# Optimization experiments

Hardware: AMD Instinct MI355X
Metric: run time of the kernel (lower is better)

## Reference

```python
import jax, jax.numpy as jnp
import numpy as np
import math

NFEAT = 1024
NHID = 512
NLAYERS = 8
LAMDA = 0.5
ALPHA = 0.1
N_DIA = 48
DIA_L = 64
N = N_DIA * DIA_L


def setup_inputs() -> dict:
    key = jax.random.key(0)
    ks = jax.random.split(key, 16)
    stdv_fc = 1.0 / math.sqrt(NFEAT)
    stdv_gc = 1.0 / math.sqrt(NHID)
    inp = {
        'a': jax.random.normal(ks[0], (N, NFEAT), jnp.float32),
        'v': jax.random.normal(ks[1], (N, NFEAT), jnp.float32),
        'l': jax.random.normal(ks[2], (N, NFEAT), jnp.float32),
        'W0': jax.random.uniform(ks[3], (NFEAT, NHID), jnp.float32, -stdv_fc, stdv_fc),
        'b0': jax.random.uniform(ks[4], (NHID,), jnp.float32, -stdv_fc, stdv_fc),
        'W1': jax.random.uniform(ks[5], (NFEAT, NHID), jnp.float32, -stdv_fc, stdv_fc),
        'b1': jax.random.uniform(ks[6], (NHID,), jnp.float32, -stdv_fc, stdv_fc),
        'W2': jax.random.uniform(ks[7], (NFEAT, NHID), jnp.float32, -stdv_fc, stdv_fc),
        'b2': jax.random.uniform(ks[8], (NHID,), jnp.float32, -stdv_fc, stdv_fc),
        'Wconv': jax.random.uniform(ks[9], (NLAYERS, NHID, NHID), jnp.float32, -stdv_gc, stdv_gc),
        'dia_len': DIA_L,  # uniform dialogue length
        'topicLabel': jnp.zeros((N,), jnp.int64),
    }
    return inp


def create_big_adj(a, v, l, dia_l):
    n = a.shape[0]
    d = n // dia_l
    feats = jnp.stack([a, v, l])                    # [3, N, F]
    x = feats.reshape(3, d, dia_l, -1)              # [3, D, L, F]
    nrm = x / jnp.sqrt(jnp.sum(x * x, axis=-1, keepdims=True))
    cos = jnp.einsum('mdif,mdjf->mdij', nrm, nrm) * 0.99999
    sim = jnp.arccos(cos)                           # [3, D, L, L]
    adj = jnp.zeros((3 * n, 3 * n), dtype=a.dtype)
    base = jnp.arange(d)[:, None, None] * dia_l     # dialogue start offsets
    rows = jnp.broadcast_to(base + jnp.arange(dia_l)[:, None], (d, dia_l, dia_l))
    cols = jnp.broadcast_to(base + jnp.arange(dia_l)[None, :], (d, dia_l, dia_l))
    for m in range(3):  # same-modality block-diagonal acos-similarity blocks
        adj = adj.at[m * n + rows, m * n + cols].set(sim[m])
    k = jnp.arange(n)
    for m in range(3):  # cross-modal: same-utterance links set to 0.99999
        for mm in range(3):
            if m != mm:
                adj = adj.at[m * n + k, mm * n + k].set(0.99999)
    dsum = jnp.sum(adj, axis=1)
    dinv = dsum ** -0.5
    return dinv[:, None] * adj * dinv[None, :]


def reference(a, v, l, W0, b0, W1, b1, W2, b2, Wconv, dia_len, topicLabel):
    relu = jax.nn.relu
    # eval mode: dropout is identity
    a_ = relu(a @ W0 + b0)
    l_ = relu(l @ W1 + b1)
    v_ = relu(v @ W2 + b2)
    x = jnp.concatenate([a_, v_, l_], axis=0)       # [3N, nhidden]
    adj = create_big_adj(a, v, l, dia_len)
    h0 = x
    h = x
    for i in range(NLAYERS):
        theta = math.log(LAMDA / (i + 1) + 1.0)
        hi = adj @ h
        support = (1.0 - ALPHA) * hi + ALPHA * h0
        h = relu(theta * (support @ Wconv[i]) + (1.0 - theta) * support)
    n = a.shape[0]
    out = jnp.concatenate([h[:n], h[n:2 * n], h[2 * n:]], axis=-1)  # [N, 3*nhidden]
    out = jnp.concatenate([l, out], axis=-1)        # use_residue
    return out
```

## Files before the change

### kernel.cpp

```cpp
#include <hip/hip_runtime.h>
#include <hip/hip_bf16.h>
#include <cmath>

#define NFEAT 1024
#define NHID  512
#define NLAYERS 8
#define NDIA 48
#define DIAL 64
#define NROW (NDIA*DIAL)
#define NROW3 (3*NROW)

typedef short bf16x8 __attribute__((ext_vector_type(8)));
typedef float f32x4  __attribute__((ext_vector_type(4)));
typedef unsigned short u16x8 __attribute__((ext_vector_type(8)));
typedef unsigned short u16x4 __attribute__((ext_vector_type(4)));
typedef unsigned short ushort_t;

__device__ __forceinline__ unsigned short f2bf(float x) {
  __hip_bfloat16 h = __float2bfloat16(x);
  return __builtin_bit_cast(unsigned short, h);
}
__device__ __forceinline__ float bf2f(unsigned short u) {
  __hip_bfloat16 h = __builtin_bit_cast(__hip_bfloat16, u);
  return __bfloat162float(h);
}

__device__ __forceinline__ void gload16(const void* g, void* l) {
  __builtin_amdgcn_global_load_lds(
      (const __attribute__((address_space(1))) void*)g,
      (__attribute__((address_space(3))) void*)l, 16, 0, 0);
}

__global__ __launch_bounds__(256) void k_prep(const float* __restrict__ a, const float* __restrict__ v,
                      const float* __restrict__ l, ushort_t* __restrict__ Abuf,
                      float* __restrict__ invn) {
  int gid = blockIdx.x * 256 + threadIdx.x;
  int row = gid >> 6, lane = gid & 63;
  int m = row / NROW, r = row % NROW;
  const float* src = (m == 0 ? a : (m == 1 ? v : l)) + (size_t)r * NFEAT;
  float4 x[4];
  float s = 0.f;
#pragma unroll
  for (int q = 0; q < 4; ++q) {
    x[q] = *reinterpret_cast<const float4*>(src + lane * 4 + q * 256);
    s += x[q].x*x[q].x + x[q].y*x[q].y + x[q].z*x[q].z + x[q].w*x[q].w;
  }
#pragma unroll
  for (int off = 32; off; off >>= 1) s += __shfl_xor(s, off);
  if (lane == 0) invn[row] = rsqrtf(s);
  ushort_t* da = Abuf + (size_t)row * NFEAT;
#pragma unroll
  for (int q = 0; q < 4; ++q) {
    u16x4 oa;
    oa[0] = f2bf(x[q].x); oa[1] = f2bf(x[q].y); oa[2] = f2bf(x[q].z); oa[3] = f2bf(x[q].w);
    *reinterpret_cast<u16x4*>(da + lane * 4 + q * 256) = oa;
  }
}

__global__ __launch_bounds__(256) void k_simm(const ushort_t* __restrict__ Ab,
                      const float* __restrict__ invn,
                      ushort_t* __restrict__ Sbf, float* __restrict__ dinv) {
  __shared__ short Xs[2][4096];
  __shared__ float simS[64][73];
  __shared__ float invS[64];
  int blk = blockIdx.x;
  const ushort_t* Xb = Ab + (size_t)blk * 64 * NFEAT;
  int t = threadIdx.x, w = t >> 6, lane = t & 63;
  if (t < 64) invS[t] = invn[blk * 64 + t];
  f32x4 acc[4] = {};

#define STAGE_SIM(b, k0) do { \
    _Pragma("unroll") \
    for (int q = 0; q < 2; ++q) { \
      int f_ = t * 8 + q * 2048; \
      int row_ = f_ >> 6; \
      int col_ = (f_ & 63) ^ ((row_ & 7) << 3); \
      gload16(Xb + (size_t)row_ * NFEAT + (k0) + col_, (void*)(Xs[b] + q * 2048 + w * 512)); \
    } } while (0)

  STAGE_SIM(0, 0);
  __syncthreads();
  for (int it = 0; it < 16; ++it) {
    int cur = it & 1;
    if (it < 15) STAGE_SIM(cur ^ 1, (it + 1) * 64);
    const char* base = (const char*)Xs[cur];
#pragma unroll
    for (int ks = 0; ks < 2; ++ks) {
      int koff = ks * 32 + (lane >> 4) * 8;
      int arow = w * 16 + (lane & 15);
      bf16x8 af = *(const bf16x8*)(base + (((arow << 7) + (koff << 1)) ^ ((arow & 7) << 4)));
#pragma unroll
      for (int j = 0; j < 4; ++j) {
        int brow = j * 16 + (lane & 15);
        bf16x8 bf = *(const bf16x8*)(base + (((brow << 7) + (koff << 1)) ^ ((brow & 7) << 4)));
        acc[j] = __builtin_amdgcn_mfma_f32_16x16x32_bf16(af, bf, acc[j], 0, 0, 0);
      }
    }
    __syncthreads();
  }
#undef STAGE_SIM

#pragma unroll
  for (int j = 0; j < 4; ++j)
#pragma unroll
    for (int e = 0; e < 4; ++e) {
      int r = w * 16 + (lane >> 4) * 4 + e;
      int c = j * 16 + (lane & 15);
      float cc = acc[j][e] * invS[r] * invS[c] * 0.99999f;
      cc = fminf(fmaxf(cc, -0.99999f), 0.99999f);
      simS[r][c] = acosf(cc);
    }
  __syncthreads();
  if (t < 64) {
    float s = 0.f;
#pragma unroll 8
    for (int c = 0; c < 64; ++c) s += simS[t][c];
    float di = rsqrtf(s + 1.99998f);
    simS[t][64] = di;
    dinv[blk * 64 + t] = di;
  }
  __syncthreads();
  ushort_t* Sb = Sbf + (size_t)blk * 4096;
#pragma unroll
  for (int q = 0; q < 2; ++q) {
    int idx = t * 8 + q * 2048;
    int i = idx >> 6, j0 = idx & 63;
    float di = simS[i][64];
    u16x8 o;
#pragma unroll
    for (int e = 0; e < 8; ++e)
      o[e] = f2bf(simS[i][j0 + e] * di * simS[j0 + e][64]);
    *reinterpret_cast<u16x8*>(Sb + idx) = o;
  }
}

__global__ void k_cvt_w(const float* __restrict__ s0, const float* __restrict__ s1,
                        const float* __restrict__ s2, ushort_t* __restrict__ dst,
                        int K, int mode) {
  __shared__ float tile[32][33];
  int z = blockIdx.z;
  const float* src = (mode == 1) ? (s0 + (size_t)z * K * NHID)
                                 : (z == 0 ? s0 : (z == 1 ? s1 : s2));
  ushort_t* d = dst + (size_t)z * NHID * K;
  int n0 = blockIdx.x * 32, k0 = blockIdx.y * 32;
  int tx = threadIdx.x & 31, ty = threadIdx.x >> 5;
#pragma unroll
  for (int q = 0; q < 4; ++q)
    tile[ty + q * 8][tx] = src[(size_t)(k0 + ty + q * 8) * NHID + n0 + tx];
  __syncthreads();
#pragma unroll
  for (int q = 0; q < 4; ++q)
    d[(size_t)(n0 + ty + q * 8) * K + k0 + tx] = f2bf(tile[tx][ty + q * 8]);
}

template<int EPI>
__global__ __launch_bounds__(256) void k_gemm_mfma(
    const ushort_t* __restrict__ A, const ushort_t* __restrict__ B,
    const float* __restrict__ ba, const float* __restrict__ bv, const float* __restrict__ bl,
    const ushort_t* __restrict__ sup, ushort_t* __restrict__ C, ushort_t* __restrict__ C2,
    int K, float theta) {
  __shared__ short As[2][128 * 64];
  __shared__ short Bs[2][64 * 64];
  int t = threadIdx.x;
  int w = t >> 6, lane = t & 63;
  int bm = blockIdx.x * 128, bn = blockIdx.y * 64;
  const float* bias = ba;
  if (EPI == 0) {
    int band = bm / NROW;
    B += (size_t)band * NHID * K;
    bias = (band == 0 ? ba : (band == 1 ? bv : bl));
  }
  const ushort_t* Ab = A + (size_t)bm * K;
  const ushort_t* Bb = B + (size_t)bn * K;
  int wr = (w >> 1) * 64, wc = (w & 1) * 32;
  f32x4 acc[4][2] = {};

#define STAGE_G(b, k0) do { \
    _Pragma("unroll") \
    for (int q = 0; q < 4; ++q) { \
      int f_ = t * 8 + q * 2048; int row_ = f_ >> 6; \
      int col_ = (f_ & 63) ^ ((row_ & 7) << 3); \
      gload16(Ab + (size_t)row_ * K + (k0) + col_, (void*)(As[b] + q * 2048 + w * 512)); } \
    _Pragma("unroll") \
    for (int q = 0; q < 2; ++q) { \
      int f_ = t * 8 + q * 2048; int row_ = f_ >> 6; \
      int col_ = (f_ & 63) ^ ((row_ & 7) << 3); \
      gload16(Bb + (size_t)row_ * K + (k0) + col_, (void*)(Bs[b] + q * 2048 + w * 512)); } \
  } while (0)

  STAGE_G(0, 0);
  __syncthreads();
  int T = K >> 6;
  for (int s = 0; s < T; ++s) {
    int cur = s & 1;
    if (s + 1 < T) STAGE_G(cur ^ 1, (s + 1) * 64);
    const char* ab = (const char*)As[cur];
    const char* bb = (const char*)Bs[cur];
#pragma unroll
    for (int ks = 0; ks < 2; ++ks) {
      bf16x8 af[4], bfr[2];
#pragma unroll
      for (int i = 0; i < 4; ++i) {
        int arow = wr + i * 16 + (lane & 15);
        int abo = (arow << 7) + ((ks * 32 + (lane >> 4) * 8) << 1);
        af[i] = *reinterpret_cast<const bf16x8*>(ab + (abo ^ ((arow & 7) << 4)));
      }
#pragma unroll
      for (int j = 0; j < 2; ++j) {
        int brow = wc + j * 16 + (lane & 15);
        int bbo = (brow << 7) + ((ks * 32 + (lane >> 4) * 8) << 1);
        bfr[j] = *reinterpret_cast<const bf16x8*>(bb + (bbo ^ ((brow & 7) << 4)));
      }
#pragma unroll
      for (int i = 0; i < 4; ++i)
#pragma unroll
        for (int j = 0; j < 2; ++j)
          acc[i][j] = __builtin_amdgcn_mfma_f32_16x16x32_bf16(af[i], bfr[j], acc[i][j], 0, 0, 0);
    }
    __syncthreads();
  }
#undef STAGE_G

#pragma unroll
  for (int i = 0; i < 4; ++i) {
#pragma unroll
    for (int jf = 0; jf < 2; ++jf) {
      int r0 = bm + wr + i * 16 + (lane >> 4) * 4;
      int c  = bn + wc + jf * 16 + (lane & 15);
#pragma unroll
      for (int j = 0; j < 4; ++j) {
        int r = r0 + j;
        float val = acc[i][jf][j];
        if (EPI == 0) {
          val = fmaxf(val + bias[c], 0.f);
          unsigned short o = f2bf(val);
          C[(size_t)r * NHID + c] = o;
          C2[(size_t)r * NHID + c] = o;
        } else {
          float s = bf2f(sup[(size_t)r * NHID + c]);
          val = fmaxf(theta * val + (1.f - theta) * s, 0.f);
          C[(size_t)r * NHID + c] = f2bf(val);
        }
      }
    }
  }
}

__global__ __launch_bounds__(256) void k_adj(const ushort_t* __restrict__ Sbf,
                      const ushort_t* __restrict__ h, const ushort_t* __restrict__ h0,
                      const float* __restrict__ dinv, ushort_t* __restrict__ sup) {
  __shared__ char ldsb[52224];
  short* Ss = (short*)ldsb;
  short (*Ht)[72] = (short (*)[72])(ldsb + 24576);
  float (*supF)[68] = (float (*)[68])ldsb;
  int d = blockIdx.x, c0 = blockIdx.y * 64;
  int t = threadIdx.x, w = t >> 6, lane = t & 63;
#pragma unroll
  for (int q = 0; q < 6; ++q) {
    int f = t * 8 + q * 2048;
    int mod = f >> 12, rem = f & 4095;
    int row = rem >> 6;
    int col = (rem & 63) ^ ((row & 7) << 3);
    gload16(Sbf + ((size_t)(mod * NDIA + d)) * 4096 + row * 64 + col,
            (void*)(Ss + q * 2048 + w * 512));
  }
#pragma unroll
  for (int q = 0; q < 6; ++q) {
    int idx = t + q * 256;
    int mod = idx >> 9, rem = idx & 511;
    int j = rem >> 3, n0 = (rem & 7) * 8;
    int key = rem & 7;
    u16x8 hv = *reinterpret_cast<const u16x8*>(
        h + ((size_t)(mod * NROW + d * 64 + j)) * NHID + c0 + n0);
    int js = j ^ (key << 3);
#pragma unroll
    for (int e = 0; e < 8; ++e) Ht[mod * 64 + n0 + e][js] = hv[e];
  }
  __syncthreads();
  f32x4 acc[3][4] = {};
#pragma unroll
  for (int m = 0; m < 3; ++m)
#pragma unroll
    for (int ks = 0; ks < 2; ++ks) {
      int koff = ks * 32 + (lane >> 4) * 8;
      int arow = w * 16 + (lane & 15);
      bf16x8 af = *(const bf16x8*)((const char*)Ss + m * 8192 +
                    (((arow << 7) + (koff << 1)) ^ ((arow & 7) << 4)));
#pragma unroll
      for (int j = 0; j < 4; ++j) {
        int n = j * 16 + (lane & 15);
        int koff_s = koff ^ (((n >> 3) & 7) << 3);
        bf16x8 bf = *(const bf16x8*)(&Ht[m * 64 + n][koff_s]);
        acc[m][j] = __builtin_amdgcn_mfma_f32_16x16x32_bf16(af, bf, acc[m][j], 0, 0, 0);
      }
    }
  __syncthreads();
#pragma unroll
  for (int m = 0; m < 3; ++m)
#pragma unroll
    for (int j = 0; j < 4; ++j)
#pragma unroll
      for (int e = 0; e < 4; ++e)
        supF[m * 64 + w * 16 + (lane >> 4) * 4 + e][j * 16 + (lane & 15)] = acc[m][j][e];
  __syncthreads();
  int r = t >> 2, cc0 = (t & 3) * 16;
  int u = d * 64 + r;
  float dv[3] = {dinv[u], dinv[NROW + u], dinv[2 * NROW + u]};
#pragma unroll
  for (int m = 0; m < 3; ++m) {
    int mm1 = (m + 1) % 3, mm2 = (m + 2) % 3;
    int g = m * NROW + u;
    float c1 = 0.99999f * dv[m] * dv[mm1];
    float c2 = 0.99999f * dv[m] * dv[mm2];
    const ushort_t* p1 = h + ((size_t)(mm1 * NROW + u)) * NHID + c0 + cc0;
    const ushort_t* p2 = h + ((size_t)(mm2 * NROW + u)) * NHID + c0 + cc0;
    const ushort_t* pz = h0 + (size_t)g * NHID + c0 + cc0;
    ushort_t* po = sup + (size_t)g * NHID + c0 + cc0;
#pragma unroll
    for (int half = 0; half < 2; ++half) {
      u16x8 h1 = *reinterpret_cast<const u16x8*>(p1 + half * 8);
      u16x8 h2 = *reinterpret_cast<const u16x8*>(p2 + half * 8);
      u16x8 hz = *reinterpret_cast<const u16x8*>(pz + half * 8);
      u16x8 o;
#pragma unroll
      for (int e = 0; e < 8; ++e) {
        float val = 0.9f * (supF[m * 64 + r][cc0 + half * 8 + e]
                    + c1 * bf2f(h1[e]) + c2 * bf2f(h2[e]))
                  + 0.1f * bf2f(hz[e]);
        o[e] = f2bf(val);
      }
      *reinterpret_cast<u16x8*>(po + half * 8) = o;
    }
  }
}

__global__ void k_out(const float* __restrict__ l, const ushort_t* __restrict__ h,
                      float* __restrict__ out) {
  int idx = blockIdx.x * blockDim.x + threadIdx.x;
  int i = idx / 640;
  int c4 = (idx % 640) * 4;
  float4 val;
  if (c4 < 1024) {
    val = *reinterpret_cast<const float4*>(l + (size_t)i * NFEAT + c4);
  } else {
    int cc = c4 - 1024;
    int m = cc >> 9, c = cc & 511;
    u16x4 hv = *reinterpret_cast<const u16x4*>(h + ((size_t)m * NROW + i) * NHID + c);
    val.x = bf2f(hv[0]); val.y = bf2f(hv[1]); val.z = bf2f(hv[2]); val.w = bf2f(hv[3]);
  }
  *reinterpret_cast<float4*>(out + (size_t)i * 2560 + c4) = val;
}

extern "C" void kernel_launch(void* const* d_in, const int* in_sizes, int n_in,
                              void* d_out, int out_size, void* d_ws, size_t ws_size,
                              hipStream_t stream) {
  const float* a  = (const float*)d_in[0];
  const float* v  = (const float*)d_in[1];
  const float* l  = (const float*)d_in[2];
  const float* W0 = (const float*)d_in[3];
  const float* b0 = (const float*)d_in[4];
  const float* W1 = (const float*)d_in[5];
  const float* b1 = (const float*)d_in[6];
  const float* W2 = (const float*)d_in[7];
  const float* b2 = (const float*)d_in[8];
  const float* Wc = (const float*)d_in[9];
  float* out = (float*)d_out;

  const size_t SZ = (size_t)NROW3 * NHID;
  const size_t XSZ = (size_t)3 * NROW * NFEAT;
  char* ws = (char*)d_ws;
  ushort_t* Abuf = (ushort_t*)ws;  ws += XSZ * 2;
  ushort_t* h0   = (ushort_t*)ws;  ws += SZ * 2;
  ushort_t* h    = (ushort_t*)ws;  ws += SZ * 2;
  ushort_t* sup  = (ushort_t*)ws;  ws += SZ * 2;
  ushort_t* Wtfc = (ushort_t*)ws;  ws += (size_t)3 * NHID * NFEAT * 2;
  ushort_t* Wct  = (ushort_t*)ws;  ws += (size_t)NLAYERS * NHID * NHID * 2;
  ushort_t* Sbf  = (ushort_t*)ws;  ws += (size_t)144 * 4096 * 2;
  float* dinv    = (float*)ws;     ws += (size_t)NROW3 * 4;
  float* invn    = (float*)ws;

  k_prep<<<NROW3 / 4, 256, 0, stream>>>(a, v, l, Abuf, invn);
  k_cvt_w<<<dim3(NHID / 32, NFEAT / 32, 3), 256, 0, stream>>>(W0, W2, W1, Wtfc, NFEAT, 0);
  k_cvt_w<<<dim3(NHID / 32, NHID / 32, NLAYERS), 256, 0, stream>>>(Wc, nullptr, nullptr, Wct, NHID, 1);
  k_simm<<<3 * NDIA, 256, 0, stream>>>(Abuf, invn, Sbf, dinv);

  k_gemm_mfma<0><<<dim3(NROW3 / 128, NHID / 64), 256, 0, stream>>>(
      Abuf, Wtfc, b0, b2, b1, nullptr, h0, h, NFEAT, 0.f);

  for (int i = 0; i < NLAYERS; ++i) {
    float theta = (float)std::log(0.5 / (i + 1) + 1.0);
    k_adj<<<dim3(NDIA, NHID / 64), 256, 0, stream>>>(Sbf, h, h0, dinv, sup);
    k_gemm_mfma<1><<<dim3(NROW3 / 128, NHID / 64), 256, 0, stream>>>(
        sup, Wct + (size_t)i * NHID * NHID, nullptr, nullptr, nullptr, sup, h, nullptr, NHID, theta);
  }

  k_out<<<(NROW * 2560 / 4) / 256, 256, 0, stream>>>(l, h, out);
}
```

Before: 229.7 us.

## Use smaller 64x64 tiles for per-layer GEMM and prefetch adj epilogue loads

Splits the templated GEMM into a dedicated FC kernel and a new per-layer GEMM with 64x64 tiles, so the 9216x512x512 layer GEMM launches twice as many blocks (1152 instead of 576) for better occupancy across CUs. In the adjacency kernel, the global loads for the cross-modal and h0 residual terms are issued before the MFMA phase, so their latency overlaps with compute. The cost is more register pressure from the prefetched vectors, and lower per-block data reuse in the smaller GEMM tiles.

```diff
diff --git a/kernel.cpp b/kernel.cpp
--- a/kernel.cpp
+++ b/kernel.cpp
@@ -153,23 +153,19 @@
     d[(size_t)(n0 + ty + q * 8) * K + k0 + tx] = f2bf(tile[tx][ty + q * 8]);
 }
 
-template<int EPI>
-__global__ __launch_bounds__(256) void k_gemm_mfma(
+__global__ __launch_bounds__(256) void k_fc(
     const ushort_t* __restrict__ A, const ushort_t* __restrict__ B,
     const float* __restrict__ ba, const float* __restrict__ bv, const float* __restrict__ bl,
-    const ushort_t* __restrict__ sup, ushort_t* __restrict__ C, ushort_t* __restrict__ C2,
-    int K, float theta) {
+    ushort_t* __restrict__ C, ushort_t* __restrict__ C2) {
   __shared__ short As[2][128 * 64];
   __shared__ short Bs[2][64 * 64];
+  const int K = NFEAT;
   int t = threadIdx.x;
   int w = t >> 6, lane = t & 63;
   int bm = blockIdx.x * 128, bn = blockIdx.y * 64;
-  const float* bias = ba;
-  if (EPI == 0) {
-    int band = bm / NROW;
-    B += (size_t)band * NHID * K;
-    bias = (band == 0 ? ba : (band == 1 ? bv : bl));
-  }
+  int band = bm / NROW;
+  B += (size_t)band * NHID * K;
+  const float* bias = (band == 0 ? ba : (band == 1 ? bv : bl));
   const ushort_t* Ab = A + (size_t)bm * K;
   const ushort_t* Bb = B + (size_t)bn * K;
   int wr = (w >> 1) * 64, wc = (w & 1) * 32;
@@ -190,7 +186,7 @@
 
   STAGE_G(0, 0);
   __syncthreads();
-  int T = K >> 6;
+  const int T = K >> 6;
   for (int s = 0; s < T; ++s) {
     int cur = s & 1;
     if (s + 1 < T) STAGE_G(cur ^ 1, (s + 1) * 64);
@@ -230,18 +226,75 @@
 #pragma unroll
       for (int j = 0; j < 4; ++j) {
         int r = r0 + j;
-        float val = acc[i][jf][j];
-        if (EPI == 0) {
-          val = fmaxf(val + bias[c], 0.f);
-          unsigned short o = f2bf(val);
-          C[(size_t)r * NHID + c] = o;
-          C2[(size_t)r * NHID + c] = o;
-        } else {
-          float s = bf2f(sup[(size_t)r * NHID + c]);
-          val = fmaxf(theta * val + (1.f - theta) * s, 0.f);
-          C[(size_t)r * NHID + c] = f2bf(val);
-        }
-      }
+        float val = fmaxf(acc[i][jf][j] + bias[c], 0.f);
+        unsigned short o = f2bf(val);
+        C[(size_t)r * NHID + c] = o;
+        C2[(size_t)r * NHID + c] = o;
+      }
+    }
+  }
+}
+
+__global__ __launch_bounds__(256) void k_gemm2(
+    const ushort_t* __restrict__ A, const ushort_t* __restrict__ B,
+    const ushort_t* __restrict__ sup_ep, ushort_t* __restrict__ C, float theta) {
+  __shared__ short As[2][64 * 64];
+  __shared__ short Bs[2][64 * 64];
+  const int K = NHID;
+  int t = threadIdx.x, w = t >> 6, lane = t & 63;
+  int bm = blockIdx.x * 64, bn = blockIdx.y * 64;
+  const ushort_t* Ab = A + (size_t)bm * K;
+  const ushort_t* Bb = B + (size_t)bn * K;
+  f32x4 acc[4] = {};
+
+#define STAGE_2(b, k0) do { \
+    _Pragma("unroll") \
+    for (int q = 0; q < 2; ++q) { \
+      int f_ = t * 8 + q * 2048; int row_ = f_ >> 6; \
+      int col_ = (f_ & 63) ^ ((row_ & 7) << 3); \
+      gload16(Ab + (size_t)row_ * K + (k0) + col_, (void*)(As[b] + q * 2048 + w * 512)); } \
+    _Pragma("unroll") \
+    for (int q = 0; q < 2; ++q) { \
+      int f_ = t * 8 + q * 2048; int row_ = f_ >> 6; \
+      int col_ = (f_ & 63) ^ ((row_ & 7) << 3); \
+      gload16(Bb + (size_t)row_ * K + (k0) + col_, (void*)(Bs[b] + q * 2048 + w * 512)); } \
+  } while (0)
+
+  STAGE_2(0, 0);
+  __syncthreads();
+  const int T = K >> 6;
+  for (int s = 0; s < T; ++s) {
+    int cur = s & 1;
+    if (s + 1 < T) STAGE_2(cur ^ 1, (s + 1) * 64);
+    const char* ab = (const char*)As[cur];
+    const char* bb = (const char*)Bs[cur];
+#pragma unroll
+    for (int ks = 0; ks < 2; ++ks) {
+      int koff = ks * 32 + (lane >> 4) * 8;
+      int arow = w * 16 + (lane & 15);
+      bf16x8 af = *(const bf16x8*)(ab + (((arow << 7) + (koff << 1)) ^ ((arow & 7) << 4)));
+#pragma unroll
+      for (int j = 0; j < 4; ++j) {
+        int brow = j * 16 + (lane & 15);
+        bf16x8 bfr = *(const bf16x8*)(bb + (((brow << 7) + (koff << 1)) ^ ((brow & 7) << 4)));
+        acc[j] = __builtin_amdgcn_mfma_f32_16x16x32_bf16(af, bfr, acc[j], 0, 0, 0);
+      }
+    }
+    __syncthreads();
+  }
+#undef STAGE_2
+
+  float omt = 1.f - theta;
+#pragma unroll
+  for (int j = 0; j < 4; ++j) {
+    int c = bn + j * 16 + (lane & 15);
+    int r0 = bm + w * 16 + (lane >> 4) * 4;
+#pragma unroll
+    for (int e = 0; e < 4; ++e) {
+      int r = r0 + e;
+      float sv = bf2f(sup_ep[(size_t)r * NHID + c]);
+      float val = fmaxf(theta * acc[j][e] + omt * sv, 0.f);
+      C[(size_t)r * NHID + c] = f2bf(val);
     }
   }
 }
@@ -276,6 +329,23 @@
 #pragma unroll
     for (int e = 0; e < 8; ++e) Ht[mod * 64 + n0 + e][js] = hv[e];
   }
+  int r = t >> 2, cc0 = (t & 3) * 16;
+  int u = d * 64 + r;
+  float dv[3] = {dinv[u], dinv[NROW + u], dinv[2 * NROW + u]};
+  u16x8 pre[3][3][2];
+#pragma unroll
+  for (int m = 0; m < 3; ++m) {
+    int mm1 = (m + 1) % 3, mm2 = (m + 2) % 3;
+    const ushort_t* p1 = h + ((size_t)(mm1 * NROW + u)) * NHID + c0 + cc0;
+    const ushort_t* p2 = h + ((size_t)(mm2 * NROW + u)) * NHID + c0 + cc0;
+    const ushort_t* pz = h0 + ((size_t)(m * NROW + u)) * NHID + c0 + cc0;
+    pre[m][0][0] = *reinterpret_cast<const u16x8*>(p1);
+    pre[m][0][1] = *reinterpret_cast<const u16x8*>(p1 + 8);
+    pre[m][1][0] = *reinterpret_cast<const u16x8*>(p2);
+    pre[m][1][1] = *reinterpret_cast<const u16x8*>(p2 + 8);
+    pre[m][2][0] = *reinterpret_cast<const u16x8*>(pz);
+    pre[m][2][1] = *reinterpret_cast<const u16x8*>(pz + 8);
+  }
   __syncthreads();
   f32x4 acc[3][4] = {};
 #pragma unroll
@@ -303,30 +373,21 @@
       for (int e = 0; e < 4; ++e)
         supF[m * 64 + w * 16 + (lane >> 4) * 4 + e][j * 16 + (lane & 15)] = acc[m][j][e];
   __syncthreads();
-  int r = t >> 2, cc0 = (t & 3) * 16;
-  int u = d * 64 + r;
-  float dv[3] = {dinv[u], dinv[NROW + u], dinv[2 * NROW + u]};
 #pragma unroll
   for (int m = 0; m < 3; ++m) {
     int mm1 = (m + 1) % 3, mm2 = (m + 2) % 3;
     int g = m * NROW + u;
     float c1 = 0.99999f * dv[m] * dv[mm1];
     float c2 = 0.99999f * dv[m] * dv[mm2];
-    const ushort_t* p1 = h + ((size_t)(mm1 * NROW + u)) * NHID + c0 + cc0;
-    const ushort_t* p2 = h + ((size_t)(mm2 * NROW + u)) * NHID + c0 + cc0;
-    const ushort_t* pz = h0 + (size_t)g * NHID + c0 + cc0;
     ushort_t* po = sup + (size_t)g * NHID + c0 + cc0;
 #pragma unroll
     for (int half = 0; half < 2; ++half) {
-      u16x8 h1 = *reinterpret_cast<const u16x8*>(p1 + half * 8);
-      u16x8 h2 = *reinterpret_cast<const u16x8*>(p2 + half * 8);
-      u16x8 hz = *reinterpret_cast<const u16x8*>(pz + half * 8);
       u16x8 o;
 #pragma unroll
       for (int e = 0; e < 8; ++e) {
         float val = 0.9f * (supF[m * 64 + r][cc0 + half * 8 + e]
-                    + c1 * bf2f(h1[e]) + c2 * bf2f(h2[e]))
-                  + 0.1f * bf2f(hz[e]);
+                    + c1 * bf2f(pre[m][0][half][e]) + c2 * bf2f(pre[m][1][half][e]))
+                  + 0.1f * bf2f(pre[m][2][half][e]);
         o[e] = f2bf(val);
       }
       *reinterpret_cast<u16x8*>(po + half * 8) = o;
@@ -384,14 +445,13 @@
   k_cvt_w<<<dim3(NHID / 32, NHID / 32, NLAYERS), 256, 0, stream>>>(Wc, nullptr, nullptr, Wct, NHID, 1);
   k_simm<<<3 * NDIA, 256, 0, stream>>>(Abuf, invn, Sbf, dinv);
 
-  k_gemm_mfma<0><<<dim3(NROW3 / 128, NHID / 64), 256, 0, stream>>>(
-      Abuf, Wtfc, b0, b2, b1, nullptr, h0, h, NFEAT, 0.f);
+  k_fc<<<dim3(NROW3 / 128, NHID / 64), 256, 0, stream>>>(Abuf, Wtfc, b0, b2, b1, h0, h);
 
   for (int i = 0; i < NLAYERS; ++i) {
     float theta = (float)std::log(0.5 / (i + 1) + 1.0);
     k_adj<<<dim3(NDIA, NHID / 64), 256, 0, stream>>>(Sbf, h, h0, dinv, sup);
-    k_gemm_mfma<1><<<dim3(NROW3 / 128, NHID / 64), 256, 0, stream>>>(
-        sup, Wct + (size_t)i * NHID * NHID, nullptr, nullptr, nullptr, sup, h, nullptr, NHID, theta);
+    k_gemm2<<<dim3(NROW3 / 64, NHID / 64), 256, 0, stream>>>(
+        sup, Wct + (size_t)i * NHID * NHID, sup, h, theta);
   }
 
   k_out<<<(NROW * 2560 / 4) / 256, 256, 0, stream>>>(l, h, out);
```

Result: slower. 266.0 us (+15.8%).
